# Kernel tuning notes

Hardware: AMD Instinct MI355X
Metric: run time of the kernel (lower is better)

The kernel has to match this reference:

```python
import jax, jax.numpy as jnp
import numpy as np

E = 1024
H = 16
D = E // H  # head_dim = 64
B = 2
S = 2048


def setup_inputs() -> dict:
    key = jax.random.key(0)
    ks = jax.random.split(key, 8)
    sc = 0.02
    return {
        "x": jax.random.normal(ks[0], (B, S, E), jnp.float32),
        "rotation_params": jax.random.normal(ks[1], (E, E), jnp.float32) * sc,
        "entangle_params": jax.random.normal(ks[2], (E, E), jnp.float32) * sc,
        "qkv_w": jax.random.normal(ks[3], (3 * E, E), jnp.float32) * sc,
        "qkv_b": jax.random.normal(ks[4], (3 * E,), jnp.float32) * sc,
        "out_w": jax.random.normal(ks[5], (E, E), jnp.float32) * sc,
        "out_b": jax.random.normal(ks[6], (E,), jnp.float32) * sc,
    }


def reference(x, rotation_params, entangle_params, qkv_w, qkv_b, out_w, out_b):
    b, s, _ = x.shape
    # qkv projection (torch Linear: x @ W.T + b)
    qkv = jnp.einsum('bse,fe->bsf', x, qkv_w) + qkv_b
    q, k, v = jnp.split(qkv, 3, axis=-1)
    # extra rotation / entangle matmuls on q and k
    q = jnp.matmul(q, rotation_params)
    k = jnp.matmul(k, entangle_params)
    # split heads: (b, h, s, d)
    q = q.reshape(b, s, H, D).transpose(0, 2, 1, 3)
    k = k.reshape(b, s, H, D).transpose(0, 2, 1, 3)
    v = v.reshape(b, s, H, D).transpose(0, 2, 1, 3)
    scores = jnp.einsum('bhqd,bhkd->bhqk', q, k) / np.sqrt(D).astype(np.float32)
    attn = jax.nn.softmax(scores, axis=-1)  # dropout p=0.0 -> identity
    out = jnp.einsum('bhqk,bhkd->bhqd', attn, v)
    out = out.transpose(0, 2, 1, 3).reshape(b, s, E)
    out = jnp.einsum('bse,fe->bsf', out, out_w) + out_b
    return out + x
```

## Files before the change

### kernel.cpp

```cpp
#include <hip/hip_runtime.h>

#define US unsigned short
#define UC unsigned char

typedef __bf16 bf16x8 __attribute__((ext_vector_type(8)));
typedef float f32x4 __attribute__((ext_vector_type(4)));
typedef unsigned int u32x4 __attribute__((ext_vector_type(4)));
typedef unsigned short u16x4 __attribute__((ext_vector_type(4)));
typedef unsigned int uint2v __attribute__((ext_vector_type(2)));

#define ALPHA_Q 0.180336880111f

#if __has_builtin(__builtin_amdgcn_exp2f)
#define EXP2F(x) __builtin_amdgcn_exp2f(x)
#else
#define EXP2F(x) __expf(0.69314718f * (x))
#endif

static __device__ __forceinline__ US f2bf(float f) {
    union { float f; unsigned u; } v; v.f = f;
    unsigned r = v.u + 0x7fffu + ((v.u >> 16) & 1u);
    return (US)(r >> 16);
}
static __device__ __forceinline__ float bf2f(US h) {
    union { unsigned u; float f; } v; v.u = ((unsigned)h) << 16;
    return v.f;
}
static __device__ __forceinline__ f32x4 mfma16(bf16x8 a, bf16x8 b, f32x4 c) {
    return __builtin_amdgcn_mfma_f32_16x16x32_bf16(a, b, c, 0, 0, 0);
}
static __device__ __forceinline__ f32x4 mfma_fp8(long long a, long long b, f32x4 c) {
    return __builtin_amdgcn_mfma_f32_16x16x32_fp8_fp8(a, b, c, 0, 0, 0);
}
static __device__ __forceinline__ void gload16(const US* g, US* l) {
    __builtin_amdgcn_global_load_lds(
        (const __attribute__((address_space(1))) void*)g,
        (__attribute__((address_space(3))) void*)l, 16, 0, 0);
}
static __device__ __forceinline__ void gload16b(const UC* g, UC* l) {
    __builtin_amdgcn_global_load_lds(
        (const __attribute__((address_space(1))) void*)g,
        (__attribute__((address_space(3))) void*)l, 16, 0, 0);
}
static __device__ __forceinline__ void stf(float* p, float v) { *p = v; }
static __device__ __forceinline__ void stf(US* p, float v) { *p = f2bf(v); }

__global__ __launch_bounds__(256) void prep(
    const float* __restrict__ x, US* __restrict__ xb,
    const float* __restrict__ qkvw, US* __restrict__ wv,
    const float* __restrict__ outw, US* __restrict__ wo,
    const float* __restrict__ Rm, US* __restrict__ rt,
    const float* __restrict__ Em, US* __restrict__ et,
    US* __restrict__ wqT, US* __restrict__ wkT,
    const float* __restrict__ qkvb, float* __restrict__ b3)
{
    __shared__ float t[64][65];
    const int bx = blockIdx.x;
    if (bx < 6144) {
        int i = bx * 256 + threadIdx.x;
        const float* s; US* d; int j;
        if (i < 1048576) { s = x; d = xb; j = i; }
        else if (i < 1310720) { s = qkvw + (size_t)2048 * 1024; d = wv; j = i - 1048576; }
        else { s = outw; d = wo; j = i - 1310720; }
        f32x4 v = ((const f32x4*)s)[j];
        u16x4 o;
        o.x = f2bf(v.x); o.y = f2bf(v.y); o.z = f2bf(v.z); o.w = f2bf(v.w);
        ((u16x4*)d)[j] = o;
    } else if (bx < 7168) {
        int r = bx - 6144;
        int z = r >> 8, xy = r & 255, tbx = xy & 15, tby = xy >> 4;
        const float* ip; US* op;
        switch (z) {
            case 0: ip = Rm; op = rt; break;
            case 1: ip = Em; op = et; break;
            case 2: ip = qkvw; op = wqT; break;
            default: ip = qkvw + (size_t)1024 * 1024; op = wkT; break;
        }
        int bc = tbx * 64, br = tby * 64;
        int lx = threadIdx.x & 63, y4 = threadIdx.x >> 6;
#pragma unroll
        for (int i = 0; i < 16; ++i) {
            int rr = i * 4 + y4;
            t[rr][lx] = ip[(size_t)(br + rr) * 1024 + bc + lx];
        }
        __syncthreads();
#pragma unroll
        for (int i = 0; i < 16; ++i) {
            int c = i * 4 + y4;
            op[(size_t)(bc + c) * 1024 + br + lx] = f2bf(t[lx][c]);
        }
    } else if (bx < 7296) {
        float (*red)[64] = (float(*)[64])t;
        const int bb = bx - 7168;
        const int tid = threadIdx.x, wave = tid >> 6, lane = tid & 63;
        const int nc = bb & 31, jc = bb >> 5;
        const int n0 = nc * 64, n = n0 + lane;
        const float* M = (n0 < 1024) ? Rm : Em;
        const float* bv = qkvb + ((n0 < 1024) ? 0 : 1024);
        const int nn = (n0 < 1024) ? n : n - 1024;
        float s = 0.f;
        const int j0 = jc * 256 + wave * 64;
#pragma unroll 8
        for (int j = 0; j < 64; ++j)
            s += bv[j0 + j] * M[(size_t)(j0 + j) * 1024 + nn];
        red[wave][lane] = s;
        __syncthreads();
        if (wave == 0) {
            float tt = red[0][lane] + red[1][lane] + red[2][lane] + red[3][lane];
            atomicAdd(&b3[n], (n0 < 1024) ? tt * ALPHA_Q : tt);
        }
    } else {
        int i = (bx - 7296) * 256 + threadIdx.x;
        b3[2048 + i] = qkvb[2048 + i];
    }
}

template <typename TO>
__global__ __launch_bounds__(256) void gemm_nt(
    const US* __restrict__ A, const US* __restrict__ Bm,
    TO* __restrict__ C, const float* __restrict__ bias,
    const float* __restrict__ resid, float alpha,
    int M, int N, int K, int lda, int ldb, int ldc)
{
    __shared__ __align__(16) US sA[128 * 32];
    __shared__ __align__(16) US sB[128 * 32];
    const int tid = threadIdx.x;
    const int wave = tid >> 6, lane = tid & 63;
    const int r16 = lane & 15, q4 = lane >> 4;
    const int wm = (wave >> 1) * 64, wn = (wave & 1) * 64;

    const int srow = wave * 32 + (lane >> 2);
    const int sg = lane & 3;
    const US* aptr = A + (size_t)(blockIdx.x * 128 + srow) * lda + sg * 8;
    const US* bptr = Bm + (size_t)(blockIdx.y * 128 + srow) * ldb + sg * 8;
    US* lA = sA + (wave * 32) * 32;
    US* lB = sB + (wave * 32) * 32;

    f32x4 acc[4][4];
#pragma unroll
    for (int i = 0; i < 4; ++i)
#pragma unroll
        for (int j = 0; j < 4; ++j) acc[i][j] = (f32x4){0.f, 0.f, 0.f, 0.f};

    for (int k0 = 0; k0 < K; k0 += 32) {
        gload16(aptr + k0, lA);
        gload16(aptr + (size_t)16 * lda + k0, lA + 16 * 32);
        gload16(bptr + k0, lB);
        gload16(bptr + (size_t)16 * ldb + k0, lB + 16 * 32);
        __syncthreads();
        bf16x8 af[4], bfr[4];
#pragma unroll
        for (int i = 0; i < 4; ++i)
            af[i] = *(const bf16x8*)&sA[(wm + i * 16 + r16) * 32 + q4 * 8];
#pragma unroll
        for (int j = 0; j < 4; ++j)
            bfr[j] = *(const bf16x8*)&sB[(wn + j * 16 + r16) * 32 + q4 * 8];
#pragma unroll
        for (int i = 0; i < 4; ++i)
#pragma unroll
            for (int j = 0; j < 4; ++j) acc[i][j] = mfma16(af[i], bfr[j], acc[i][j]);
        __syncthreads();
    }

#pragma unroll
    for (int j = 0; j < 4; ++j) {
        int col = blockIdx.y * 128 + wn + j * 16 + r16;
        float bv = bias ? bias[col] : 0.f;
#pragma unroll
        for (int i = 0; i < 4; ++i) {
#pragma unroll
            for (int rr = 0; rr < 4; ++rr) {
                int row = blockIdx.x * 128 + wm + i * 16 + q4 * 4 + rr;
                float v = acc[i][j][rr] * alpha + bv;
                if (resid) v += resid[(size_t)row * ldc + col];
                stf(&C[(size_t)row * ldc + col], v);
            }
        }
    }
}

__global__ __launch_bounds__(256) void gemm_qkv(
    const US* __restrict__ A, const US* __restrict__ Bm,
    const float* __restrict__ bias,
    US* __restrict__ qk, UC* __restrict__ vt)
{
    __shared__ __align__(16) US sA[128 * 32];
    __shared__ __align__(16) US sB[128 * 32];
    const int tid = threadIdx.x;
    const int wave = tid >> 6, lane = tid & 63;
    const int r16 = lane & 15, q4 = lane >> 4;
    const int wm = (wave >> 1) * 64, wn = (wave & 1) * 64;

    const int srow = wave * 32 + (lane >> 2);
    const int sg = lane & 3;
    const US* aptr = A + (size_t)(blockIdx.x * 128 + srow) * 1024 + sg * 8;
    const US* bptr = Bm + (size_t)(blockIdx.y * 128 + srow) * 1024 + sg * 8;
    US* lA = sA + (wave * 32) * 32;
    US* lB = sB + (wave * 32) * 32;

    f32x4 acc[4][4];
#pragma unroll
    for (int i = 0; i < 4; ++i)
#pragma unroll
        for (int j = 0; j < 4; ++j) acc[i][j] = (f32x4){0.f, 0.f, 0.f, 0.f};

    for (int k0 = 0; k0 < 1024; k0 += 32) {
        gload16(aptr + k0, lA);
        gload16(aptr + (size_t)16 * 1024 + k0, lA + 16 * 32);
        gload16(bptr + k0, lB);
        gload16(bptr + (size_t)16 * 1024 + k0, lB + 16 * 32);
        __syncthreads();
        bf16x8 af[4], bfr[4];
#pragma unroll
        for (int i = 0; i < 4; ++i)
            af[i] = *(const bf16x8*)&sA[(wm + i * 16 + r16) * 32 + q4 * 8];
#pragma unroll
        for (int j = 0; j < 4; ++j)
            bfr[j] = *(const bf16x8*)&sB[(wn + j * 16 + r16) * 32 + q4 * 8];
#pragma unroll
        for (int i = 0; i < 4; ++i)
#pragma unroll
            for (int j = 0; j < 4; ++j) acc[i][j] = mfma16(af[i], bfr[j], acc[i][j]);
        __syncthreads();
    }

    if (blockIdx.y < 16) {
#pragma unroll
        for (int j = 0; j < 4; ++j) {
            int col = blockIdx.y * 128 + wn + j * 16 + r16;
            float bv = bias[col];
#pragma unroll
            for (int i = 0; i < 4; ++i)
#pragma unroll
                for (int rr = 0; rr < 4; ++rr) {
                    int row = blockIdx.x * 128 + wm + i * 16 + q4 * 4 + rr;
                    qk[(size_t)row * 2048 + col] = f2bf(acc[i][j][rr] + bv);
                }
        }
    } else {
#pragma unroll
        for (int j = 0; j < 4; ++j) {
            int col = blockIdx.y * 128 + wn + j * 16 + r16;
            float bv = bias[col];
            int f = col - 2048;
#pragma unroll
            for (int i = 0; i < 4; ++i) {
                int row0 = blockIdx.x * 128 + wm + i * 16 + q4 * 4;
                int b = row0 >> 11, s0 = row0 & 2047;
                int dw = __builtin_amdgcn_cvt_pk_fp8_f32(
                    acc[i][j][0] + bv, acc[i][j][1] + bv, 0, false);
                dw = __builtin_amdgcn_cvt_pk_fp8_f32(
                    acc[i][j][2] + bv, acc[i][j][3] + bv, dw, true);
                *(unsigned int*)&vt[((size_t)(b * 1024 + f)) * 2048 + s0] = (unsigned)dw;
            }
        }
    }
}

__global__ __launch_bounds__(256) void gemm_fold(
    const US* __restrict__ rt, const US* __restrict__ wqT,
    const US* __restrict__ et, const US* __restrict__ wkT,
    US* __restrict__ comb)
{
    __shared__ __align__(16) US sA[64 * 32];
    __shared__ __align__(16) US sB[64 * 32];
    const US* A; const US* Bm; US* C; float alpha;
    if (blockIdx.z == 0) { A = rt; Bm = wqT; C = comb; alpha = ALPHA_Q; }
    else { A = et; Bm = wkT; C = comb + (size_t)1024 * 1024; alpha = 1.0f; }

    const int tid = threadIdx.x;
    const int wave = tid >> 6, lane = tid & 63;
    const int r16 = lane & 15, q4 = lane >> 4;
    const int wm = (wave >> 1) * 32, wn = (wave & 1) * 32;

    const int srow = wave * 16 + (lane >> 2);
    const int sg = lane & 3;
    const US* aptr = A + (size_t)(blockIdx.x * 64 + srow) * 1024 + sg * 8;
    const US* bptr = Bm + (size_t)(blockIdx.y * 64 + srow) * 1024 + sg * 8;
    US* lA = sA + (wave * 16) * 32;
    US* lB = sB + (wave * 16) * 32;

    f32x4 acc[2][2];
#pragma unroll
    for (int i = 0; i < 2; ++i)
#pragma unroll
        for (int j = 0; j < 2; ++j) acc[i][j] = (f32x4){0.f, 0.f, 0.f, 0.f};

    for (int k0 = 0; k0 < 1024; k0 += 32) {
        gload16(aptr + k0, lA);
        gload16(bptr + k0, lB);
        __syncthreads();
        bf16x8 af[2], bfr[2];
#pragma unroll
        for (int i = 0; i < 2; ++i)
            af[i] = *(const bf16x8*)&sA[(wm + i * 16 + r16) * 32 + q4 * 8];
#pragma unroll
        for (int j = 0; j < 2; ++j)
            bfr[j] = *(const bf16x8*)&sB[(wn + j * 16 + r16) * 32 + q4 * 8];
#pragma unroll
        for (int i = 0; i < 2; ++i)
#pragma unroll
            for (int j = 0; j < 2; ++j) acc[i][j] = mfma16(af[i], bfr[j], acc[i][j]);
        __syncthreads();
    }

#pragma unroll
    for (int j = 0; j < 2; ++j) {
        int col = blockIdx.y * 64 + wn + j * 16 + r16;
#pragma unroll
        for (int i = 0; i < 2; ++i)
#pragma unroll
            for (int rr = 0; rr < 4; ++rr) {
                int row = blockIdx.x * 64 + wm + i * 16 + q4 * 4 + rr;
                C[(size_t)row * 1024 + col] = f2bf(acc[i][j][rr] * alpha);
            }
    }
}

__global__ __launch_bounds__(128) void attn_kernel(
    const US* __restrict__ qk, const UC* __restrict__ vt, US* __restrict__ out)
{
    __shared__ __align__(16) US sK[2 * 64 * 64];
    __shared__ __align__(16) UC sV[2 * 64 * 64];
    __shared__ __align__(16) UC sP[2 * 64 * 72];
    const int tid = threadIdx.x;
    const int wave = tid >> 6, lane = tid & 63;
    const int r16 = lane & 15, q4 = lane >> 4;
    const int bid = blockIdx.x;
    const int pair = (bid & 7) * 4 + ((bid >> 3) & 3);
    const int qc = bid >> 5;
    const int h = pair & 15, b = pair >> 4;
    const int qrow0 = qc * 128 + wave * 64;
    const int c7 = r16 & 7, c3 = r16 & 3;

    const US* qbase = qk + ((size_t)(b * 2048 + qrow0)) * 2048 + h * 64;
    bf16x8 qa[4][2];
#pragma unroll
    for (int qt = 0; qt < 4; ++qt)
#pragma unroll
        for (int kh = 0; kh < 2; ++kh)
            qa[qt][kh] = *(const bf16x8*)(qbase + (size_t)(qt * 16 + r16) * 2048 + kh * 32 + q4 * 8);

    f32x4 o[4][4];
    float lacc[4];
#pragma unroll
    for (int dt = 0; dt < 4; ++dt)
#pragma unroll
        for (int qt = 0; qt < 4; ++qt) o[dt][qt] = (f32x4){0.f, 0.f, 0.f, 0.f};
#pragma unroll
    for (int qt = 0; qt < 4; ++qt) lacc[qt] = 0.f;

    const int l8 = lane >> 3;
    const US* kg = qk + ((size_t)(b * 2048 + wave * 32 + l8)) * 2048 + 1024 + h * 64
                 + (((lane & 7) ^ l8)) * 8;
    const int r4 = lane >> 2;
    const UC* vg = vt + ((size_t)((b * 16 + h) * 64 + wave * 32 + r4)) * 2048
                 + (((lane & 3) ^ (r4 & 3))) * 16;
    UC* pl = sP + wave * 4608;

#define STAGE(kc, buf) do {                                                    \
        US* dK = sK + (buf) * 4096 + (wave * 32) * 64;                         \
        UC* dV = sV + (buf) * 4096 + (wave * 32) * 64;                         \
        _Pragma("unroll")                                                      \
        for (int c = 0; c < 4; ++c)                                            \
            gload16(kg + (size_t)((kc) + c * 8) * 2048, dK + c * 8 * 64);      \
        _Pragma("unroll")                                                      \
        for (int c = 0; c < 2; ++c)                                            \
            gload16b(vg + (size_t)(c * 16) * 2048 + (kc), dV + c * 16 * 64);   \
    } while (0)

    STAGE(0, 0);
    STAGE(64, 1);
    for (int it = 0; it < 32; ++it) {
        const int buf = it & 1;
        if (it < 31) asm volatile("s_waitcnt vmcnt(6)" ::: "memory");
        else         asm volatile("s_waitcnt vmcnt(0)" ::: "memory");
        asm volatile("s_barrier" ::: "memory");
        const US* K0 = sK + buf * 4096;
        const UC* V0 = sV + buf * 4096;

#pragma unroll
        for (int kt = 0; kt < 4; ++kt) {
            bf16x8 kf0 = *(const bf16x8*)&K0[(kt * 16 + r16) * 64 + ((0 + q4) ^ c7) * 8];
            bf16x8 kf1 = *(const bf16x8*)&K0[(kt * 16 + r16) * 64 + ((4 + q4) ^ c7) * 8];
#pragma unroll
            for (int qt = 0; qt < 4; ++qt) {
                f32x4 st = mfma16(kf0, qa[qt][0], (f32x4){0.f, 0.f, 0.f, 0.f});
                st = mfma16(kf1, qa[qt][1], st);
                float p0 = EXP2F(st[0]), p1 = EXP2F(st[1]);
                float p2 = EXP2F(st[2]), p3 = EXP2F(st[3]);
                lacc[qt] += (p0 + p1) + (p2 + p3);
                int dw = __builtin_amdgcn_cvt_pk_fp8_f32(p0, p1, 0, false);
                dw = __builtin_amdgcn_cvt_pk_fp8_f32(p2, p3, dw, true);
                *(unsigned int*)&pl[(qt * 16 + r16) * 72 + kt * 16 + q4 * 4] = (unsigned)dw;
            }
        }
        asm volatile("s_waitcnt lgkmcnt(0)" ::: "memory");

        long long pa[4][2];
#pragma unroll
        for (int qt = 0; qt < 4; ++qt)
#pragma unroll
            for (int ks = 0; ks < 2; ++ks)
                pa[qt][ks] = *(const long long*)&pl[(qt * 16 + r16) * 72 + ks * 32 + q4 * 8];
#pragma unroll
        for (int dt = 0; dt < 4; ++dt)
#pragma unroll
            for (int ks = 0; ks < 2; ++ks) {
                int g8 = ks * 4 + q4;
                long long vf = *(const long long*)&V0[(dt * 16 + r16) * 64
                              + (((g8 >> 1) ^ c3) << 4) + ((g8 & 1) << 3)];
#pragma unroll
                for (int qt = 0; qt < 4; ++qt)
                    o[dt][qt] = mfma_fp8(vf, pa[qt][ks], o[dt][qt]);
            }

        asm volatile("s_barrier" ::: "memory");
        if (it < 30) STAGE((it + 2) * 64, buf);
    }
#undef STAGE

#pragma unroll
    for (int qt = 0; qt < 4; ++qt) {
        float l = lacc[qt];
        l += __shfl_xor(l, 16);
        l += __shfl_xor(l, 32);
        const float inv = 1.0f / l;
        const size_t row = (size_t)(b * 2048 + qrow0 + qt * 16 + r16);
#pragma unroll
        for (int dt = 0; dt < 4; ++dt) {
            uint2v w;
            w.x = (unsigned)f2bf(o[dt][qt][0] * inv) | ((unsigned)f2bf(o[dt][qt][1] * inv) << 16);
            w.y = (unsigned)f2bf(o[dt][qt][2] * inv) | ((unsigned)f2bf(o[dt][qt][3] * inv) << 16);
            *(uint2v*)&out[row * 1024 + h * 64 + dt * 16 + q4 * 4] = w;
        }
    }
}

extern "C" void kernel_launch(void* const* d_in, const int* in_sizes, int n_in,
                              void* d_out, int out_size, void* d_ws, size_t ws_size,
                              hipStream_t stream)
{
    const float* x    = (const float*)d_in[0];
    const float* Rm   = (const float*)d_in[1];
    const float* Em   = (const float*)d_in[2];
    const float* qkvw = (const float*)d_in[3];
    const float* qkvb = (const float*)d_in[4];
    const float* outw = (const float*)d_in[5];
    const float* outb = (const float*)d_in[6];
    float* outp = (float*)d_out;

    US* ws    = (US*)d_ws;
    US* xb    = ws;
    US* rt    = xb   + (size_t)4096 * 1024;
    US* et    = rt   + (size_t)1024 * 1024;
    US* wqT   = et   + (size_t)1024 * 1024;
    US* wkT   = wqT  + (size_t)1024 * 1024;
    US* wo    = wkT  + (size_t)1024 * 1024;
    US* comb  = wo   + (size_t)1024 * 1024;
    US* qkvq  = comb + (size_t)3072 * 1024;
    US* ao    = qkvq + (size_t)4096 * 2048;
    UC* vt    = (UC*)(ao + (size_t)4096 * 1024);
    float* b3 = (float*)(vt + (size_t)2048 * 2048);

    hipMemsetAsync(b3, 0, 2048 * sizeof(float), stream);
    prep<<<dim3(7300), dim3(256), 0, stream>>>(
        x, xb, qkvw, comb + (size_t)2048 * 1024, outw, wo,
        Rm, rt, Em, et, wqT, wkT, qkvb, b3);
    gemm_fold<<<dim3(16, 16, 2), dim3(256), 0, stream>>>(rt, wqT, et, wkT, comb);
    gemm_qkv<<<dim3(32, 24), dim3(256), 0, stream>>>(xb, comb, b3, qkvq, vt);
    attn_kernel<<<dim3(512), dim3(128), 0, stream>>>(qkvq, vt, ao);
    gemm_nt<float><<<dim3(32, 8), dim3(256), 0, stream>>>(ao, wo, outp, outb, x, 1.0f,
                                                          4096, 1024, 1024, 1024, 1024, 1024);
}
```

Before: 253.5 us.

## Shrink GEMM M-tiles to 64 and split attention key blocks across four waves

The QKV and output GEMMs now use 64-row tiles instead of 128, doubling the number of blocks to fill more compute units. The attention kernel moves from 128-thread blocks, where each wave owned 64 query rows, to 256-thread blocks over 64 query rows. Each wave now handles one 16-key slice of every 64-key chunk, and the softmax row sums are combined across waves in shared memory. V is written in a permuted order so each wave can read its P·V fragments with a single 16-byte load. The trade-off is less data reuse per block, an extra barrier per iteration, and the loss of the two-deep prefetch overlap.

```diff
diff --git a/kernel.cpp b/kernel.cpp
--- a/kernel.cpp
+++ b/kernel.cpp
@@ -116,47 +116,44 @@
 }
 
 template <typename TO>
-__global__ __launch_bounds__(256) void gemm_nt(
+__global__ __launch_bounds__(256) void gemm_nt64(
     const US* __restrict__ A, const US* __restrict__ Bm,
     TO* __restrict__ C, const float* __restrict__ bias,
-    const float* __restrict__ resid, float alpha,
+    const float* __restrict__ resid,
     int M, int N, int K, int lda, int ldb, int ldc)
 {
-    __shared__ __align__(16) US sA[128 * 32];
+    __shared__ __align__(16) US sA[64 * 32];
     __shared__ __align__(16) US sB[128 * 32];
     const int tid = threadIdx.x;
     const int wave = tid >> 6, lane = tid & 63;
     const int r16 = lane & 15, q4 = lane >> 4;
-    const int wm = (wave >> 1) * 64, wn = (wave & 1) * 64;
-
-    const int srow = wave * 32 + (lane >> 2);
-    const int sg = lane & 3;
-    const US* aptr = A + (size_t)(blockIdx.x * 128 + srow) * lda + sg * 8;
-    const US* bptr = Bm + (size_t)(blockIdx.y * 128 + srow) * ldb + sg * 8;
-    US* lA = sA + (wave * 32) * 32;
+    const int wm = (wave >> 1) * 32, wn = (wave & 1) * 64;
+
+    const US* aptr = A + (size_t)(blockIdx.x * 64 + wave * 16 + (lane >> 2)) * lda + (lane & 3) * 8;
+    const US* bptr = Bm + (size_t)(blockIdx.y * 128 + wave * 32 + (lane >> 2)) * ldb + (lane & 3) * 8;
+    US* lA = sA + (wave * 16) * 32;
     US* lB = sB + (wave * 32) * 32;
 
-    f32x4 acc[4][4];
-#pragma unroll
-    for (int i = 0; i < 4; ++i)
+    f32x4 acc[2][4];
+#pragma unroll
+    for (int i = 0; i < 2; ++i)
 #pragma unroll
         for (int j = 0; j < 4; ++j) acc[i][j] = (f32x4){0.f, 0.f, 0.f, 0.f};
 
     for (int k0 = 0; k0 < K; k0 += 32) {
         gload16(aptr + k0, lA);
-        gload16(aptr + (size_t)16 * lda + k0, lA + 16 * 32);
         gload16(bptr + k0, lB);
         gload16(bptr + (size_t)16 * ldb + k0, lB + 16 * 32);
         __syncthreads();
-        bf16x8 af[4], bfr[4];
-#pragma unroll
-        for (int i = 0; i < 4; ++i)
+        bf16x8 af[2], bfr[4];
+#pragma unroll
+        for (int i = 0; i < 2; ++i)
             af[i] = *(const bf16x8*)&sA[(wm + i * 16 + r16) * 32 + q4 * 8];
 #pragma unroll
         for (int j = 0; j < 4; ++j)
             bfr[j] = *(const bf16x8*)&sB[(wn + j * 16 + r16) * 32 + q4 * 8];
 #pragma unroll
-        for (int i = 0; i < 4; ++i)
+        for (int i = 0; i < 2; ++i)
 #pragma unroll
             for (int j = 0; j < 4; ++j) acc[i][j] = mfma16(af[i], bfr[j], acc[i][j]);
         __syncthreads();
@@ -167,11 +164,11 @@
         int col = blockIdx.y * 128 + wn + j * 16 + r16;
         float bv = bias ? bias[col] : 0.f;
 #pragma unroll
-        for (int i = 0; i < 4; ++i) {
+        for (int i = 0; i < 2; ++i) {
 #pragma unroll
             for (int rr = 0; rr < 4; ++rr) {
-                int row = blockIdx.x * 128 + wm + i * 16 + q4 * 4 + rr;
-                float v = acc[i][j][rr] * alpha + bv;
+                int row = blockIdx.x * 64 + wm + i * 16 + q4 * 4 + rr;
+                float v = acc[i][j][rr] + bv;
                 if (resid) v += resid[(size_t)row * ldc + col];
                 stf(&C[(size_t)row * ldc + col], v);
             }
@@ -184,41 +181,38 @@
     const float* __restrict__ bias,
     US* __restrict__ qk, UC* __restrict__ vt)
 {
-    __shared__ __align__(16) US sA[128 * 32];
+    __shared__ __align__(16) US sA[64 * 32];
     __shared__ __align__(16) US sB[128 * 32];
     const int tid = threadIdx.x;
     const int wave = tid >> 6, lane = tid & 63;
     const int r16 = lane & 15, q4 = lane >> 4;
-    const int wm = (wave >> 1) * 64, wn = (wave & 1) * 64;
-
-    const int srow = wave * 32 + (lane >> 2);
-    const int sg = lane & 3;
-    const US* aptr = A + (size_t)(blockIdx.x * 128 + srow) * 1024 + sg * 8;
-    const US* bptr = Bm + (size_t)(blockIdx.y * 128 + srow) * 1024 + sg * 8;
-    US* lA = sA + (wave * 32) * 32;
+    const int wm = (wave >> 1) * 32, wn = (wave & 1) * 64;
+
+    const US* aptr = A + (size_t)(blockIdx.x * 64 + wave * 16 + (lane >> 2)) * 1024 + (lane & 3) * 8;
+    const US* bptr = Bm + (size_t)(blockIdx.y * 128 + wave * 32 + (lane >> 2)) * 1024 + (lane & 3) * 8;
+    US* lA = sA + (wave * 16) * 32;
     US* lB = sB + (wave * 32) * 32;
 
-    f32x4 acc[4][4];
-#pragma unroll
-    for (int i = 0; i < 4; ++i)
+    f32x4 acc[2][4];
+#pragma unroll
+    for (int i = 0; i < 2; ++i)
 #pragma unroll
         for (int j = 0; j < 4; ++j) acc[i][j] = (f32x4){0.f, 0.f, 0.f, 0.f};
 
     for (int k0 = 0; k0 < 1024; k0 += 32) {
         gload16(aptr + k0, lA);
-        gload16(aptr + (size_t)16 * 1024 + k0, lA + 16 * 32);
         gload16(bptr + k0, lB);
         gload16(bptr + (size_t)16 * 1024 + k0, lB + 16 * 32);
         __syncthreads();
-        bf16x8 af[4], bfr[4];
-#pragma unroll
-        for (int i = 0; i < 4; ++i)
+        bf16x8 af[2], bfr[4];
+#pragma unroll
+        for (int i = 0; i < 2; ++i)
             af[i] = *(const bf16x8*)&sA[(wm + i * 16 + r16) * 32 + q4 * 8];
 #pragma unroll
         for (int j = 0; j < 4; ++j)
             bfr[j] = *(const bf16x8*)&sB[(wn + j * 16 + r16) * 32 + q4 * 8];
 #pragma unroll
-        for (int i = 0; i < 4; ++i)
+        for (int i = 0; i < 2; ++i)
 #pragma unroll
             for (int j = 0; j < 4; ++j) acc[i][j] = mfma16(af[i], bfr[j], acc[i][j]);
         __syncthreads();
@@ -230,10 +224,10 @@
             int col = blockIdx.y * 128 + wn + j * 16 + r16;
             float bv = bias[col];
 #pragma unroll
-            for (int i = 0; i < 4; ++i)
+            for (int i = 0; i < 2; ++i)
 #pragma unroll
                 for (int rr = 0; rr < 4; ++rr) {
-                    int row = blockIdx.x * 128 + wm + i * 16 + q4 * 4 + rr;
+                    int row = blockIdx.x * 64 + wm + i * 16 + q4 * 4 + rr;
                     qk[(size_t)row * 2048 + col] = f2bf(acc[i][j][rr] + bv);
                 }
         }
@@ -244,14 +238,16 @@
             float bv = bias[col];
             int f = col - 2048;
 #pragma unroll
-            for (int i = 0; i < 4; ++i) {
-                int row0 = blockIdx.x * 128 + wm + i * 16 + q4 * 4;
+            for (int i = 0; i < 2; ++i) {
+                int row0 = blockIdx.x * 64 + wm + i * 16 + q4 * 4;
                 int b = row0 >> 11, s0 = row0 & 2047;
+                int k = s0 & 63;
+                int p = (s0 & ~63) | ((k & 24) << 1) | ((k & 32) >> 2) | (k & 7);
                 int dw = __builtin_amdgcn_cvt_pk_fp8_f32(
                     acc[i][j][0] + bv, acc[i][j][1] + bv, 0, false);
                 dw = __builtin_amdgcn_cvt_pk_fp8_f32(
                     acc[i][j][2] + bv, acc[i][j][3] + bv, dw, true);
-                *(unsigned int*)&vt[((size_t)(b * 1024 + f)) * 2048 + s0] = (unsigned)dw;
+                *(unsigned int*)&vt[((size_t)(b * 1024 + f)) * 2048 + p] = (unsigned)dw;
             }
         }
     }
@@ -317,12 +313,13 @@
     }
 }
 
-__global__ __launch_bounds__(128) void attn_kernel(
+__global__ __launch_bounds__(256) void attn_kernel(
     const US* __restrict__ qk, const UC* __restrict__ vt, US* __restrict__ out)
 {
     __shared__ __align__(16) US sK[2 * 64 * 64];
     __shared__ __align__(16) UC sV[2 * 64 * 64];
-    __shared__ __align__(16) UC sP[2 * 64 * 72];
+    __shared__ __align__(16) UC sP[64 * 72];
+    __shared__ float lred[4][64];
     const int tid = threadIdx.x;
     const int wave = tid >> 6, lane = tid & 63;
     const int r16 = lane & 15, q4 = lane >> 4;
@@ -330,8 +327,8 @@
     const int pair = (bid & 7) * 4 + ((bid >> 3) & 3);
     const int qc = bid >> 5;
     const int h = pair & 15, b = pair >> 4;
-    const int qrow0 = qc * 128 + wave * 64;
-    const int c7 = r16 & 7, c3 = r16 & 3;
+    const int qrow0 = qc * 64;
+    const int c7 = r16 & 7;
 
     const US* qbase = qk + ((size_t)(b * 2048 + qrow0)) * 2048 + h * 64;
     bf16x8 qa[4][2];
@@ -341,82 +338,62 @@
         for (int kh = 0; kh < 2; ++kh)
             qa[qt][kh] = *(const bf16x8*)(qbase + (size_t)(qt * 16 + r16) * 2048 + kh * 32 + q4 * 8);
 
-    f32x4 o[4][4];
+    f32x4 o[4];
     float lacc[4];
 #pragma unroll
-    for (int dt = 0; dt < 4; ++dt)
-#pragma unroll
-        for (int qt = 0; qt < 4; ++qt) o[dt][qt] = (f32x4){0.f, 0.f, 0.f, 0.f};
-#pragma unroll
-    for (int qt = 0; qt < 4; ++qt) lacc[qt] = 0.f;
+    for (int qt = 0; qt < 4; ++qt) { o[qt] = (f32x4){0.f, 0.f, 0.f, 0.f}; lacc[qt] = 0.f; }
 
     const int l8 = lane >> 3;
-    const US* kg = qk + ((size_t)(b * 2048 + wave * 32 + l8)) * 2048 + 1024 + h * 64
-                 + (((lane & 7) ^ l8)) * 8;
+    const US* kg = qk + ((size_t)(b * 2048 + wave * 16 + l8)) * 2048 + 1024 + h * 64
+                 + ((lane & 7) ^ l8) * 8;
     const int r4 = lane >> 2;
-    const UC* vg = vt + ((size_t)((b * 16 + h) * 64 + wave * 32 + r4)) * 2048
-                 + (((lane & 3) ^ (r4 & 3))) * 16;
-    UC* pl = sP + wave * 4608;
+    const UC* vg = vt + ((size_t)((b * 16 + h) * 64 + wave * 16 + r4)) * 2048
+                 + ((lane & 3) ^ (r4 & 3)) * 16;
 
 #define STAGE(kc, buf) do {                                                    \
-        US* dK = sK + (buf) * 4096 + (wave * 32) * 64;                         \
-        UC* dV = sV + (buf) * 4096 + (wave * 32) * 64;                         \
-        _Pragma("unroll")                                                      \
-        for (int c = 0; c < 4; ++c)                                            \
-            gload16(kg + (size_t)((kc) + c * 8) * 2048, dK + c * 8 * 64);      \
-        _Pragma("unroll")                                                      \
-        for (int c = 0; c < 2; ++c)                                            \
-            gload16b(vg + (size_t)(c * 16) * 2048 + (kc), dV + c * 16 * 64);   \
+        US* dK = sK + (buf) * 4096 + (wave * 16) * 64;                         \
+        UC* dV = sV + (buf) * 4096 + (wave * 16) * 64;                         \
+        gload16(kg + (size_t)(kc) * 2048, dK);                                 \
+        gload16(kg + (size_t)((kc) + 8) * 2048, dK + 8 * 64);                  \
+        gload16b(vg + (kc), dV);                                               \
     } while (0)
 
     STAGE(0, 0);
-    STAGE(64, 1);
     for (int it = 0; it < 32; ++it) {
         const int buf = it & 1;
-        if (it < 31) asm volatile("s_waitcnt vmcnt(6)" ::: "memory");
-        else         asm volatile("s_waitcnt vmcnt(0)" ::: "memory");
+        asm volatile("s_waitcnt vmcnt(0)" ::: "memory");
         asm volatile("s_barrier" ::: "memory");
+        if (it < 31) STAGE((it + 1) * 64, buf ^ 1);
+
         const US* K0 = sK + buf * 4096;
+        bf16x8 kf0 = *(const bf16x8*)&K0[(wave * 16 + r16) * 64 + ((0 + q4) ^ c7) * 8];
+        bf16x8 kf1 = *(const bf16x8*)&K0[(wave * 16 + r16) * 64 + ((4 + q4) ^ c7) * 8];
+#pragma unroll
+        for (int qt = 0; qt < 4; ++qt) {
+            f32x4 st = mfma16(kf0, qa[qt][0], (f32x4){0.f, 0.f, 0.f, 0.f});
+            st = mfma16(kf1, qa[qt][1], st);
+            float p0 = EXP2F(st[0]), p1 = EXP2F(st[1]);
+            float p2 = EXP2F(st[2]), p3 = EXP2F(st[3]);
+            lacc[qt] += (p0 + p1) + (p2 + p3);
+            int dw = __builtin_amdgcn_cvt_pk_fp8_f32(p0, p1, 0, false);
+            dw = __builtin_amdgcn_cvt_pk_fp8_f32(p2, p3, dw, true);
+            *(unsigned int*)&sP[(qt * 16 + r16) * 72 + wave * 16 + q4 * 4] = (unsigned)dw;
+        }
+        asm volatile("s_waitcnt lgkmcnt(0)" ::: "memory");
+        asm volatile("s_barrier" ::: "memory");
+
         const UC* V0 = sV + buf * 4096;
-
-#pragma unroll
-        for (int kt = 0; kt < 4; ++kt) {
-            bf16x8 kf0 = *(const bf16x8*)&K0[(kt * 16 + r16) * 64 + ((0 + q4) ^ c7) * 8];
-            bf16x8 kf1 = *(const bf16x8*)&K0[(kt * 16 + r16) * 64 + ((4 + q4) ^ c7) * 8];
-#pragma unroll
-            for (int qt = 0; qt < 4; ++qt) {
-                f32x4 st = mfma16(kf0, qa[qt][0], (f32x4){0.f, 0.f, 0.f, 0.f});
-                st = mfma16(kf1, qa[qt][1], st);
-                float p0 = EXP2F(st[0]), p1 = EXP2F(st[1]);
-                float p2 = EXP2F(st[2]), p3 = EXP2F(st[3]);
-                lacc[qt] += (p0 + p1) + (p2 + p3);
-                int dw = __builtin_amdgcn_cvt_pk_fp8_f32(p0, p1, 0, false);
-                dw = __builtin_amdgcn_cvt_pk_fp8_f32(p2, p3, dw, true);
-                *(unsigned int*)&pl[(qt * 16 + r16) * 72 + kt * 16 + q4 * 4] = (unsigned)dw;
-            }
-        }
-        asm volatile("s_waitcnt lgkmcnt(0)" ::: "memory");
-
-        long long pa[4][2];
-#pragma unroll
-        for (int qt = 0; qt < 4; ++qt)
-#pragma unroll
-            for (int ks = 0; ks < 2; ++ks)
-                pa[qt][ks] = *(const long long*)&pl[(qt * 16 + r16) * 72 + ks * 32 + q4 * 8];
-#pragma unroll
-        for (int dt = 0; dt < 4; ++dt)
-#pragma unroll
-            for (int ks = 0; ks < 2; ++ks) {
-                int g8 = ks * 4 + q4;
-                long long vf = *(const long long*)&V0[(dt * 16 + r16) * 64
-                              + (((g8 >> 1) ^ c3) << 4) + ((g8 & 1) << 3)];
-#pragma unroll
-                for (int qt = 0; qt < 4; ++qt)
-                    o[dt][qt] = mfma_fp8(vf, pa[qt][ks], o[dt][qt]);
-            }
-
-        asm volatile("s_barrier" ::: "memory");
-        if (it < 30) STAGE((it + 2) * 64, buf);
+        u32x4 vv = *(const u32x4*)&V0[(wave * 16 + r16) * 64 + (q4 ^ (r16 & 3)) * 16];
+        long long vf0, vf1;
+        { uint2v t0 = {vv.x, vv.y}; vf0 = *(long long*)&t0; }
+        { uint2v t1 = {vv.z, vv.w}; vf1 = *(long long*)&t1; }
+#pragma unroll
+        for (int qt = 0; qt < 4; ++qt) {
+            long long pa0 = *(const long long*)&sP[(qt * 16 + r16) * 72 + q4 * 8];
+            long long pa1 = *(const long long*)&sP[(qt * 16 + r16) * 72 + 32 + q4 * 8];
+            o[qt] = mfma_fp8(vf0, pa0, o[qt]);
+            o[qt] = mfma_fp8(vf1, pa1, o[qt]);
+        }
     }
 #undef STAGE
 
@@ -425,15 +402,19 @@
         float l = lacc[qt];
         l += __shfl_xor(l, 16);
         l += __shfl_xor(l, 32);
-        const float inv = 1.0f / l;
-        const size_t row = (size_t)(b * 2048 + qrow0 + qt * 16 + r16);
-#pragma unroll
-        for (int dt = 0; dt < 4; ++dt) {
-            uint2v w;
-            w.x = (unsigned)f2bf(o[dt][qt][0] * inv) | ((unsigned)f2bf(o[dt][qt][1] * inv) << 16);
-            w.y = (unsigned)f2bf(o[dt][qt][2] * inv) | ((unsigned)f2bf(o[dt][qt][3] * inv) << 16);
-            *(uint2v*)&out[row * 1024 + h * 64 + dt * 16 + q4 * 4] = w;
-        }
+        if (q4 == 0) lred[wave][qt * 16 + r16] = l;
+    }
+    __syncthreads();
+#pragma unroll
+    for (int qt = 0; qt < 4; ++qt) {
+        int i = qt * 16 + r16;
+        float l = lred[0][i] + lred[1][i] + lred[2][i] + lred[3][i];
+        float inv = 1.0f / l;
+        size_t row = (size_t)(b * 2048 + qrow0 + qt * 16 + r16);
+        uint2v w;
+        w.x = (unsigned)f2bf(o[qt][0] * inv) | ((unsigned)f2bf(o[qt][1] * inv) << 16);
+        w.y = (unsigned)f2bf(o[qt][2] * inv) | ((unsigned)f2bf(o[qt][3] * inv) << 16);
+        *(uint2v*)&out[row * 1024 + h * 64 + wave * 16 + q4 * 4] = w;
     }
 }
 
@@ -468,8 +449,8 @@
         x, xb, qkvw, comb + (size_t)2048 * 1024, outw, wo,
         Rm, rt, Em, et, wqT, wkT, qkvb, b3);
     gemm_fold<<<dim3(16, 16, 2), dim3(256), 0, stream>>>(rt, wqT, et, wkT, comb);
-    gemm_qkv<<<dim3(32, 24), dim3(256), 0, stream>>>(xb, comb, b3, qkvq, vt);
-    attn_kernel<<<dim3(512), dim3(128), 0, stream>>>(qkvq, vt, ao);
-    gemm_nt<float><<<dim3(32, 8), dim3(256), 0, stream>>>(ao, wo, outp, outb, x, 1.0f,
-                                                          4096, 1024, 1024, 1024, 1024, 1024);
-}
+    gemm_qkv<<<dim3(64, 24), dim3(256), 0, stream>>>(xb, comb, b3, qkvq, vt);
+    attn_kernel<<<dim3(1024), dim3(256), 0, stream>>>(qkvq, vt, ao);
+    gemm_nt64<float><<<dim3(64, 8), dim3(256), 0, stream>>>(ao, wo, outp, outb, x,
+                                                            4096, 1024, 1024, 1024, 1024, 1024);
+}
```

Result: faster. 232.2 us (-8.4%).
